# Optimization experiments

Hardware: AMD Instinct MI355X
Metric: run time of the kernel (lower is better)

The kernel has to match this reference:

```python
import jax, jax.numpy as jnp
import numpy as np

B, C, H = 4, 1, 256          # batch, channels, square image size
A, P = 180, 256              # n_angles, n_detector_positions
T = int(np.ceil(np.sqrt(2.0) * H))  # samples per ray (covers image diagonal) = 363


def setup_inputs() -> dict:
    key = jax.random.key(0)
    x = jax.random.normal(key, (B, C, H, H), dtype=jnp.float32)
    # projection angles uniformly covering [0, pi)
    thetas = (jnp.pi * jnp.arange(A, dtype=jnp.float32) / A)
    # detector offsets in pixel units, centered on the image center
    positions = jnp.arange(P, dtype=jnp.float32) - (P - 1) / 2.0
    return {"x": x, "thetas": thetas, "positions": positions}


def _radon(x, thetas, positions):
    """Radon transform: line integrals along rays (theta, s) with bilinear
    sampling at unit spacing along each ray. Returns sinogram [B,C,A,P]."""
    Bc, Cc, Hh, Ww = x.shape
    cx = (Ww - 1) / 2.0
    cy = (Hh - 1) / 2.0
    t = jnp.arange(T, dtype=x.dtype) - (T - 1) / 2.0          # [T] along-ray param
    cos = jnp.cos(thetas)[:, None, None]                       # [A,1,1]
    sin = jnp.sin(thetas)[:, None, None]
    s = positions[None, :, None]                               # [1,P,1]
    tt = t[None, None, :]                                      # [1,1,T]
    # rotated ray sample coordinates, [A,P,T]
    px = cx + s * cos - tt * sin
    py = cy + s * sin + tt * cos
    x0 = jnp.floor(px)
    y0 = jnp.floor(py)
    wx = px - x0
    wy = py - y0
    x0i = x0.astype(jnp.int32)
    y0i = y0.astype(jnp.int32)

    def gather(iy, ix):
        # zero outside the image (zero-padding boundary)
        valid = (ix >= 0) & (ix < Ww) & (iy >= 0) & (iy < Hh)
        ixc = jnp.clip(ix, 0, Ww - 1)
        iyc = jnp.clip(iy, 0, Hh - 1)
        v = x[:, :, iyc, ixc]                                  # [B,C,A,P,T]
        return v * valid.astype(x.dtype)

    interp = (gather(y0i,     x0i)     * ((1.0 - wx) * (1.0 - wy))
            + gather(y0i,     x0i + 1) * (wx * (1.0 - wy))
            + gather(y0i + 1, x0i)     * ((1.0 - wx) * wy)
            + gather(y0i + 1, x0i + 1) * (wx * wy))
    return interp.sum(axis=-1)                                 # [B,C,A,P]


def reference(x, thetas, positions):
    return _radon(x, thetas, positions)
```

## Files before the change

### kernel.cpp

```cpp
#include <hip/hip_runtime.h>
#include <hip/hip_fp16.h>


#define NB   4
#define NA   180
#define NP   256
#define GANG 3
#define NSEG 4
#define NQ   4

#define IMG_DW  17802
#define RED_OFF (IMG_DW * 4)
#define SMEM_BYTES (RED_OFF + NP * NSEG * 4)

__device__ __forceinline__ unsigned pack_h2(float a, float b) {
    __half2 h = __halves2half2(__float2half_rn(a), __float2half_rn(b));
    return *reinterpret_cast<unsigned*>(&h);
}

template<int STRIDE>
__device__ __forceinline__ float ray_accum(
    const unsigned int* __restrict__ imgw,
    float bxr, float byr, float nsv, float cv,
    float xlo, float xhi, float ylo, float yhi,
    int tlo, int thi, int seg)
{
    float acc = 0.f;
    int   t  = tlo + seg;
    float pxu = fmaf((float)t - 181.0f, nsv, bxr);
    float pyu = fmaf((float)t - 181.0f, cv,  byr);
    const float dpx = 4.0f * nsv;
    const float dpy = 4.0f * cv;
    #pragma unroll 4
    for (; t < thi; t += 4) {
        float px = __builtin_amdgcn_fmed3f(pxu, xlo, xhi);
        float py = __builtin_amdgcn_fmed3f(pyu, ylo, yhi);
        pxu += dpx;
        pyu += dpy;
        const float fx = floorf(px);
        const float fy = floorf(py);
        const float wx = px - fx;
        const float wy = py - fy;
        const int ad = (int)fmaf(fy, (float)STRIDE, fx);
        const unsigned q0 = imgw[ad];
        const unsigned q1 = imgw[ad + 1];
        unsigned A = __builtin_amdgcn_perm(q1, q0, 0x05040100u);
        unsigned B = __builtin_amdgcn_perm(q1, q0, 0x07060302u);
        const __half2 hA = *reinterpret_cast<__half2*>(&A);
        const __half2 hB = *reinterpret_cast<__half2*>(&B);
        const __half2 wy2 = __half2half2(__float2half_rn(wy));
        const __half2 V = __hfma2(wy2, __hsub2(hB, hA), hA);
        const float vlo = __half2float(__low2half(V));
        const float vhi = __half2float(__high2half(V));
        acc = fmaf(wx, vhi - vlo, acc + vlo);
    }
    return acc;
}

extern "C" __global__ __launch_bounds__(1024)
void radon_fwd(const float* __restrict__ x,
               const float* __restrict__ thetas,
               const float* __restrict__ positions,
               float* __restrict__ out)
{
    extern __shared__ unsigned char smem[];
    unsigned int* imgw = (unsigned int*)smem;
    float*        red  = (float*)(smem + RED_OFF);

    const int grp = blockIdx.x;
    const int b   = blockIdx.y;
    const int qz  = blockIdx.z;
    const int a0  = grp * GANG;
    const bool regA = (a0 < 45) || (a0 >= 135);
    const int tid = threadIdx.x + (threadIdx.y << 8);
    const float* __restrict__ xb = x + b * 65536;

    if (regA) {
        for (int d = tid; d < 67 * 261; d += 1024) {
            const int r = d / 261, c = d - r * 261;
            const int gr = 64 * qz + r - 1;
            const int gc = c - 2;
            const bool gok = (gc >= 0) & (gc < 256);
            const float v0 = (gok && gr >= 0   && gr < 256) ? xb[gr * 256 + gc]       : 0.f;
            const float v1 = (gok && gr >= -1  && gr < 255) ? xb[(gr + 1) * 256 + gc] : 0.f;
            imgw[d] = pack_h2(v0, v1);
        }
    } else {
        for (int d = tid; d < 258 * 69; d += 1024) {
            const int r = d / 69, c = d - r * 69;
            const int gr = r - 1;
            const int gc = 64 * qz + c - 2;
            const bool gok = (gc >= 0) & (gc < 256);
            const float v0 = (gok && gr >= 0  && gr < 256) ? xb[gr * 256 + gc]       : 0.f;
            const float v1 = (gok && gr >= -1 && gr < 255) ? xb[(gr + 1) * 256 + gc] : 0.f;
            imgw[d] = pack_h2(v0, v1);
        }
    }
    __syncthreads();

    float xlo, xhi, ylo, yhi;
    if (regA) { xlo = 1.f; xhi = 258.f;       ylo = 0.f; yhi = 66.f;  }
    else      { xlo = 1.f; xhi = 66.984375f;  ylo = 0.f; yhi = 257.f; }

    const int   p   = threadIdx.x;
    const int   seg = threadIdx.y;
    const float s   = positions[p];

    float accs[GANG];
    for (int g = 0; g < GANG; ++g) {
        const float th  = thetas[a0 + g];
        const float cv  = cosf(th);
        const float sv  = sinf(th);
        const float nsv = -sv;
        const float bx2 = fmaf(s, cv, 129.5f);
        const float by1 = fmaf(s, sv, 128.5f);

        const float slope = regA ? cv : nsv;
        const float base  = regA ? by1 : bx2;
        const float off   = regA ? 1.0f : 2.0f;
        float S[3];
        #pragma unroll
        for (int i = 0; i < 3; ++i) {
            const float thr = 64.0f * (float)(i + 1) + off;
            const float ts  = 181.0f + (thr - base) / slope;
            const float Sf  = (slope > 0.f) ? ceilf(ts) : (floorf(ts) + 1.0f);
            S[i] = fmaxf(0.f, fminf(364.f, Sf));
        }
        int lo, hi;
        if (slope > 0.f) {
            lo = (qz == 0) ? 0   : (int)S[qz - 1];
            hi = (qz == 3) ? 364 : (int)S[qz];
        } else {
            lo = (qz == 3) ? 0   : (int)S[qz];
            hi = (qz == 0) ? 364 : (int)S[qz - 1];
        }

        const float msx = (fabsf(sv) < 1e-7f) ? copysignf(1e-7f, sv) : sv;
        const float mcy = (fabsf(cv) < 1e-7f) ? copysignf(1e-7f, cv) : cv;
        const float invx = -1.0f / msx;
        const float invy =  1.0f / mcy;
        const float ux1 = (1.0f   - bx2) * invx;
        const float ux2 = (258.0f - bx2) * invx;
        const float uy1 = (0.0f   - by1) * invy;
        const float uy2 = (257.0f - by1) * invy;
        const float ulo = fmaxf(fminf(ux1, ux2), fminf(uy1, uy2));
        const float uhi = fminf(fmaxf(ux1, ux2), fmaxf(uy1, uy2));
        const float tbf = ceilf(ulo + 181.0f) - 1.0f;
        const float tef = floorf(uhi + 181.0f) + 2.0f;
        const int tb = (int)fmaxf((float)lo, fminf(364.0f, tbf));
        const int te = (int)fminf((float)hi, fmaxf(0.0f,  tef));

        const float bxr = regA ? bx2 : (bx2 - 64.0f * (float)qz);
        const float byr = regA ? (by1 - 64.0f * (float)qz) : by1;
        accs[g] = regA
            ? ray_accum<261>(imgw, bxr, byr, nsv, cv, xlo, xhi, ylo, yhi, tb, te, seg)
            : ray_accum< 69>(imgw, bxr, byr, nsv, cv, xlo, xhi, ylo, yhi, tb, te, seg);
    }

    for (int g = 0; g < GANG; ++g) {
        __syncthreads();
        red[(seg << 8) + p] = accs[g];
        __syncthreads();
        if (seg == 0) {
            float r4 = red[p] + red[256 + p] + red[512 + p] + red[768 + p];
            atomicAdd(&out[b * (NA * NP) + (a0 + g) * NP + p], r4);
        }
    }
}

extern "C" void kernel_launch(void* const* d_in, const int* in_sizes, int n_in,
                              void* d_out, int out_size, void* d_ws, size_t ws_size,
                              hipStream_t stream) {
    const float* x         = (const float*)d_in[0];
    const float* thetas    = (const float*)d_in[1];
    const float* positions = (const float*)d_in[2];
    float* out = (float*)d_out;

    hipFuncSetAttribute((const void*)radon_fwd,
                        hipFuncAttributeMaxDynamicSharedMemorySize, SMEM_BYTES);

    hipMemsetAsync(d_out, 0, (size_t)out_size * sizeof(float), stream);

    dim3 grid(NA / GANG, NB, NQ);
    dim3 block(NP, NSEG);
    radon_fwd<<<grid, block, SMEM_BYTES, stream>>>(x, thetas, positions, out);
}
```

Baseline: 125.6 us.

## Split image into two halves per block with vectorized float4 staging

```diff
diff --git a/kernel.cpp b/kernel.cpp
--- a/kernel.cpp
+++ b/kernel.cpp
@@ -7,10 +7,13 @@
 #define NP   256
 #define GANG 3
 #define NSEG 4
-#define NQ   4
-
-#define IMG_DW  17802
-#define RED_OFF (IMG_DW * 4)
+
+#define STRIDE_A 261
+#define ROWS_A   135
+#define STRIDE_B 138
+#define ROWS_B   259
+#define IMG_DW   (ROWS_B * STRIDE_B)
+#define RED_OFF  (IMG_DW * 4)
 #define SMEM_BYTES (RED_OFF + NP * NSEG * 4)
 
 __device__ __forceinline__ unsigned pack_h2(float a, float b) {
@@ -67,40 +70,71 @@
     unsigned int* imgw = (unsigned int*)smem;
     float*        red  = (float*)(smem + RED_OFF);
 
-    const int grp = blockIdx.x;
-    const int b   = blockIdx.y;
-    const int qz  = blockIdx.z;
-    const int a0  = grp * GANG;
+    const int grp  = blockIdx.x;
+    const int b    = blockIdx.y;
+    const int half = blockIdx.z;
+    const int a0   = grp * GANG;
     const bool regA = (a0 < 45) || (a0 >= 135);
     const int tid = threadIdx.x + (threadIdx.y << 8);
     const float* __restrict__ xb = x + b * 65536;
+    const float4* __restrict__ xb4 = (const float4*)xb;
+
+    for (int i = tid; i < IMG_DW; i += 1024) imgw[i] = 0u;
+    __syncthreads();
 
     if (regA) {
-        for (int d = tid; d < 67 * 261; d += 1024) {
-            const int r = d / 261, c = d - r * 261;
-            const int gr = 64 * qz + r - 1;
-            const int gc = c - 2;
-            const bool gok = (gc >= 0) & (gc < 256);
-            const float v0 = (gok && gr >= 0   && gr < 256) ? xb[gr * 256 + gc]       : 0.f;
-            const float v1 = (gok && gr >= -1  && gr < 255) ? xb[(gr + 1) * 256 + gc] : 0.f;
-            imgw[d] = pack_h2(v0, v1);
+        const int Fb = half ? 122 : -2;
+        for (int d = tid; d < ROWS_A * 64; d += 1024) {
+            const int r  = d >> 6;
+            const int j  = d & 63;
+            const int R0 = Fb + r, R1 = R0 + 1;
+            const int r0c = min(max(R0, 0), 255), r1c = min(max(R1, 0), 255);
+            const float4 f0 = xb4[r0c * 64 + j];
+            const float4 f1 = xb4[r1c * 64 + j];
+            const bool m0 = ((unsigned)R0 < 256u), m1 = ((unsigned)R1 < 256u);
+            const float t0x = m0 ? f0.x : 0.f, t0y = m0 ? f0.y : 0.f,
+                        t0z = m0 ? f0.z : 0.f, t0w = m0 ? f0.w : 0.f;
+            const float t1x = m1 ? f1.x : 0.f, t1y = m1 ? f1.y : 0.f,
+                        t1z = m1 ? f1.z : 0.f, t1w = m1 ? f1.w : 0.f;
+            const int cb = r * STRIDE_A + 4 * j + 2;
+            imgw[cb + 0] = pack_h2(t0x, t1x);
+            imgw[cb + 1] = pack_h2(t0y, t1y);
+            imgw[cb + 2] = pack_h2(t0z, t1z);
+            imgw[cb + 3] = pack_h2(t0w, t1w);
         }
     } else {
-        for (int d = tid; d < 258 * 69; d += 1024) {
-            const int r = d / 69, c = d - r * 69;
-            const int gr = r - 1;
-            const int gc = 64 * qz + c - 2;
-            const bool gok = (gc >= 0) & (gc < 256);
-            const float v0 = (gok && gr >= 0  && gr < 256) ? xb[gr * 256 + gc]       : 0.f;
-            const float v1 = (gok && gr >= -1 && gr < 255) ? xb[(gr + 1) * 256 + gc] : 0.f;
-            imgw[d] = pack_h2(v0, v1);
+        for (int d = tid; d < ROWS_B * 34; d += 1024) {
+            const int r = d / 34;
+            const int j = d - r * 34;
+            const int R0 = r - 2, R1 = r - 1;
+            const int r0c = min(max(R0, 0), 255), r1c = min(max(R1, 0), 255);
+            const int col4 = j + (half ? 30 : 0);
+            const float4 f0 = xb4[r0c * 64 + col4];
+            const float4 f1 = xb4[r1c * 64 + col4];
+            const bool m0 = ((unsigned)R0 < 256u), m1 = ((unsigned)R1 < 256u);
+            const float t0x = m0 ? f0.x : 0.f, t0y = m0 ? f0.y : 0.f,
+                        t0z = m0 ? f0.z : 0.f, t0w = m0 ? f0.w : 0.f;
+            const float t1x = m1 ? f1.x : 0.f, t1y = m1 ? f1.y : 0.f,
+                        t1z = m1 ? f1.z : 0.f, t1w = m1 ? f1.w : 0.f;
+            const int cb = r * STRIDE_B + 4 * j + (half ? 0 : 2);
+            imgw[cb + 0] = pack_h2(t0x, t1x);
+            imgw[cb + 1] = pack_h2(t0y, t1y);
+            imgw[cb + 2] = pack_h2(t0z, t1z);
+            imgw[cb + 3] = pack_h2(t0w, t1w);
         }
     }
     __syncthreads();
 
-    float xlo, xhi, ylo, yhi;
-    if (regA) { xlo = 1.f; xhi = 258.f;       ylo = 0.f; yhi = 66.f;  }
-    else      { xlo = 1.f; xhi = 66.984375f;  ylo = 0.f; yhi = 257.f; }
+    float xlo, xhi, ylo, yhi, CbX, CbY;
+    if (regA) {
+        xlo = 0.f; xhi = 259.0f;
+        ylo = 0.f; yhi = 134.984375f;
+        CbX = -2.f; CbY = half ? 122.f : -2.f;
+    } else {
+        xlo = 0.f; xhi = 136.984375f;
+        ylo = 0.f; yhi = 258.984375f;
+        CbX = half ? 120.f : -2.f; CbY = -2.f;
+    }
 
     const int   p   = threadIdx.x;
     const int   seg = threadIdx.y;
@@ -112,37 +146,26 @@
         const float cv  = cosf(th);
         const float sv  = sinf(th);
         const float nsv = -sv;
-        const float bx2 = fmaf(s, cv, 129.5f);
-        const float by1 = fmaf(s, sv, 128.5f);
+        const float bxI = fmaf(s, cv, 127.5f);
+        const float byI = fmaf(s, sv, 127.5f);
 
         const float slope = regA ? cv : nsv;
-        const float base  = regA ? by1 : bx2;
-        const float off   = regA ? 1.0f : 2.0f;
-        float S[3];
-        #pragma unroll
-        for (int i = 0; i < 3; ++i) {
-            const float thr = 64.0f * (float)(i + 1) + off;
-            const float ts  = 181.0f + (thr - base) / slope;
-            const float Sf  = (slope > 0.f) ? ceilf(ts) : (floorf(ts) + 1.0f);
-            S[i] = fmaxf(0.f, fminf(364.f, Sf));
-        }
-        int lo, hi;
-        if (slope > 0.f) {
-            lo = (qz == 0) ? 0   : (int)S[qz - 1];
-            hi = (qz == 3) ? 364 : (int)S[qz];
-        } else {
-            lo = (qz == 3) ? 0   : (int)S[qz];
-            hi = (qz == 0) ? 364 : (int)S[qz - 1];
-        }
+        const float base  = regA ? byI : bxI;
+        const float tstar = 181.0f + (128.0f - base) / slope;
+        const float Sf    = (slope > 0.f) ? ceilf(tstar) : (floorf(tstar) + 1.0f);
+        const int   S     = (int)fmaxf(0.f, fminf(364.f, Sf));
+        const bool  h0Low = (slope > 0.f);
+        const int lo = ((half == 0) == h0Low) ? 0 : S;
+        const int hi = ((half == 0) == h0Low) ? S : 364;
 
         const float msx = (fabsf(sv) < 1e-7f) ? copysignf(1e-7f, sv) : sv;
         const float mcy = (fabsf(cv) < 1e-7f) ? copysignf(1e-7f, cv) : cv;
         const float invx = -1.0f / msx;
         const float invy =  1.0f / mcy;
-        const float ux1 = (1.0f   - bx2) * invx;
-        const float ux2 = (258.0f - bx2) * invx;
-        const float uy1 = (0.0f   - by1) * invy;
-        const float uy2 = (257.0f - by1) * invy;
+        const float ux1 = (-2.0f  - bxI) * invx;
+        const float ux2 = (257.0f - bxI) * invx;
+        const float uy1 = (-2.0f  - byI) * invy;
+        const float uy2 = (257.0f - byI) * invy;
         const float ulo = fmaxf(fminf(ux1, ux2), fminf(uy1, uy2));
         const float uhi = fminf(fmaxf(ux1, ux2), fmaxf(uy1, uy2));
         const float tbf = ceilf(ulo + 181.0f) - 1.0f;
@@ -150,11 +173,11 @@
         const int tb = (int)fmaxf((float)lo, fminf(364.0f, tbf));
         const int te = (int)fminf((float)hi, fmaxf(0.0f,  tef));
 
-        const float bxr = regA ? bx2 : (bx2 - 64.0f * (float)qz);
-        const float byr = regA ? (by1 - 64.0f * (float)qz) : by1;
+        const float bxr = bxI - CbX;
+        const float byr = byI - CbY;
         accs[g] = regA
-            ? ray_accum<261>(imgw, bxr, byr, nsv, cv, xlo, xhi, ylo, yhi, tb, te, seg)
-            : ray_accum< 69>(imgw, bxr, byr, nsv, cv, xlo, xhi, ylo, yhi, tb, te, seg);
+            ? ray_accum<STRIDE_A>(imgw, bxr, byr, nsv, cv, xlo, xhi, ylo, yhi, tb, te, seg)
+            : ray_accum<STRIDE_B>(imgw, bxr, byr, nsv, cv, xlo, xhi, ylo, yhi, tb, te, seg);
     }
 
     for (int g = 0; g < GANG; ++g) {
@@ -181,7 +204,7 @@
 
     hipMemsetAsync(d_out, 0, (size_t)out_size * sizeof(float), stream);
 
-    dim3 grid(NA / GANG, NB, NQ);
+    dim3 grid(NA / GANG, NB, 2);
     dim3 block(NP, NSEG);
     radon_fwd<<<grid, block, SMEM_BYTES, stream>>>(x, thetas, positions, out);
 }
```

Result: faster. 116.1 us (-7.6%).
